# Kernel tuning notes

Hardware: AMD Instinct MI355X
Metric: run time of the kernel (lower is better)

The kernel has to match this reference:

```python
import jax, jax.numpy as jnp
import numpy as np

B, L, D = 16, 512, 512
NPIX, ENC_D = 196, 4096
AL, ATTR_D = 20, 300
H, DK = 8, 64
DFF = 2048
KS = 3


def _lin(x, w, b):
    return x @ w.T + b


def _ln_custom(x, a, b, eps=1e-6):
    # torch .std is unbiased (ddof=1); module divides by (std + eps)
    mean = x.mean(-1, keepdims=True)
    n = x.shape[-1]
    std = jnp.sqrt(((x - mean) ** 2).sum(-1, keepdims=True) / (n - 1))
    return a * (x - mean) / (std + eps) + b


def _ln(x, eps=1e-5):
    # fresh nn.LayerNorm each call -> gamma=1, beta=0
    mean = x.mean(-1, keepdims=True)
    var = ((x - mean) ** 2).mean(-1, keepdims=True)
    return (x - mean) / jnp.sqrt(var + eps)


def _mha(Q, K, V, mask, wq, bq, wk, bk, wv, bv, wo, bo):
    bsz = Q.shape[0]
    q = _lin(Q, wq, bq).reshape(bsz, -1, H, DK)
    k = _lin(K, wk, bk).reshape(bsz, -1, H, DK)
    v = _lin(V, wv, bv).reshape(bsz, -1, H, DK)
    scores = jnp.einsum('bqhd,bkhd->bhqk', q, k) / np.sqrt(DK).astype(np.float32)
    scores = jnp.where(mask[:, None], jnp.float32(-1e9), scores)
    attn = jax.nn.softmax(scores, axis=-1)
    ctx = jnp.einsum('bhqk,bkhd->bqhd', attn, v).reshape(bsz, -1, H * DK)
    out = _lin(ctx, wo, bo)
    return _ln(out + Q), attn


def _lstm_last(xw, w_ih, w_hh, b_ih, b_hh):
    # xw: [N, KS, D]; torch LSTM gate order i,f,g,o; return last hidden
    N = xw.shape[0]
    h = jnp.zeros((N, D), xw.dtype)
    c = jnp.zeros((N, D), xw.dtype)
    for t in range(KS):  # KS=3, unrolled
        g = xw[:, t] @ w_ih.T + b_ih + h @ w_hh.T + b_hh
        i, f, gg, o = jnp.split(g, 4, axis=-1)
        c = jax.nn.sigmoid(f) * c + jax.nn.sigmoid(i) * jnp.tanh(gg)
        h = jax.nn.sigmoid(o) * jnp.tanh(c)
    return h


def _local_rnn(x, conv_w, conv_b, w_ih, w_hh, b_ih, b_hh):
    a, b = jnp.split(x, 2, axis=-1)
    x = a * jax.nn.sigmoid(b)          # GLU: [B,L,512] -> [B,L,256]
    x = x @ conv_w.T + conv_b          # 1x1 conv == linear: -> [B,L,512]
    bsz, l, d = x.shape
    xp = jnp.pad(x, ((0, 0), (KS - 1, 0), (0, 0)))
    win = jnp.stack([xp[:, i:i + l] for i in range(KS)], axis=2)  # [B,L,KS,512]
    h = _lstm_last(win.reshape(-1, KS, d), w_ih, w_hh, b_ih, b_hh)
    return h.reshape(bsz, l, d)


def _forward(dec_inputs, enc_outputs, attr_out,
             dec_self_attn_mask, dec_enc_attn_mask, attr_dec_attn_mask,
             rnn_norm_a, rnn_norm_b, conv_w, conv_b,
             lstm_w_ih, lstm_w_hh, lstm_b_ih, lstm_b_hh,
             sa_wq, sa_bq, sa_wk, sa_bk, sa_wv, sa_bv, sa_wo, sa_bo,
             ea_wq, ea_bq, ea_wk, ea_bk, ea_wv, ea_bv, ea_wo, ea_bo,
             aa_wq, aa_bq, aa_wk, aa_bk, aa_wv, aa_bv, aa_wo, aa_bo,
             fc_w, fc_b, norm_a, norm_b, ffn_w1, ffn_b1, ffn_w2, ffn_b2):
    # LocalRNNLayer: x + local_rnn(custom_LN(x))  (dropout = eval/identity)
    x = dec_inputs + _local_rnn(_ln_custom(dec_inputs, rnn_norm_a, rnn_norm_b),
                                conv_w, conv_b, lstm_w_ih, lstm_w_hh, lstm_b_ih, lstm_b_hh)
    dec_out, self_attn = _mha(x, x, x, dec_self_attn_mask,
                              sa_wq, sa_bq, sa_wk, sa_bk, sa_wv, sa_bv, sa_wo, sa_bo)
    img, enc_attn = _mha(dec_out, enc_outputs, enc_outputs, dec_enc_attn_mask,
                         ea_wq, ea_bq, ea_wk, ea_bk, ea_wv, ea_bv, ea_wo, ea_bo)
    attr, _ = _mha(dec_out, attr_out, attr_out, attr_dec_attn_mask,
                   aa_wq, aa_bq, aa_wk, aa_bk, aa_wv, aa_bv, aa_wo, aa_bo)
    # NOTE: original concatenates img with img (faithful to source bug)
    ct = jax.nn.sigmoid(_lin(jnp.concatenate([img, img], axis=-1), fc_w, fc_b))
    y = _ln_custom(ct * jax.nn.relu(img) + (1.0 - ct) * jax.nn.relu(attr), norm_a, norm_b)
    y = _ln(_lin(jax.nn.relu(_lin(y, ffn_w1, ffn_b1)), ffn_w2, ffn_b2) + y)
    return y, self_attn, enc_attn


def setup_inputs() -> dict:
    key = jax.random.key(0)
    keys = iter(jax.random.split(key, 40))
    w = lambda shape: jax.random.normal(next(keys), shape, jnp.float32) * 0.02
    causal = jnp.broadcast_to(jnp.triu(jnp.ones((L, L), bool), 1), (B, L, L))
    inp = {
        'dec_inputs': jax.random.normal(next(keys), (B, L, D), jnp.float32),
        'enc_outputs': jax.random.normal(next(keys), (B, NPIX, ENC_D), jnp.float32),
        'attr_out': jax.random.normal(next(keys), (B, AL, ATTR_D), jnp.float32),
        'dec_self_attn_mask': causal,
        'dec_enc_attn_mask': jnp.zeros((B, L, NPIX), bool),
        'attr_dec_attn_mask': jnp.zeros((B, L, AL), bool),
        'rnn_norm_a': jnp.ones((D,), jnp.float32),
        'rnn_norm_b': jnp.zeros((D,), jnp.float32),
        'conv_w': w((D, D // 2)), 'conv_b': jnp.zeros((D,), jnp.float32),
        'lstm_w_ih': w((4 * D, D)), 'lstm_w_hh': w((4 * D, D)),
        'lstm_b_ih': jnp.zeros((4 * D,), jnp.float32), 'lstm_b_hh': jnp.zeros((4 * D,), jnp.float32),
        'sa_wq': w((H * DK, D)), 'sa_bq': jnp.zeros((H * DK,), jnp.float32),
        'sa_wk': w((H * DK, D)), 'sa_bk': jnp.zeros((H * DK,), jnp.float32),
        'sa_wv': w((H * DK, D)), 'sa_bv': jnp.zeros((H * DK,), jnp.float32),
        'sa_wo': w((D, H * DK)), 'sa_bo': jnp.zeros((D,), jnp.float32),
        'ea_wq': w((H * DK, D)), 'ea_bq': jnp.zeros((H * DK,), jnp.float32),
        'ea_wk': w((H * DK, ENC_D)), 'ea_bk': jnp.zeros((H * DK,), jnp.float32),
        'ea_wv': w((H * DK, ENC_D)), 'ea_bv': jnp.zeros((H * DK,), jnp.float32),
        'ea_wo': w((D, H * DK)), 'ea_bo': jnp.zeros((D,), jnp.float32),
        'aa_wq': w((H * DK, D)), 'aa_bq': jnp.zeros((H * DK,), jnp.float32),
        'aa_wk': w((H * DK, ATTR_D)), 'aa_bk': jnp.zeros((H * DK,), jnp.float32),
        'aa_wv': w((H * DK, ATTR_D)), 'aa_bv': jnp.zeros((H * DK,), jnp.float32),
        'aa_wo': w((D, H * DK)), 'aa_bo': jnp.zeros((D,), jnp.float32),
        'fc_w': w((D, 2 * D)), 'fc_b': jnp.zeros((D,), jnp.float32),
        'norm_a': jnp.ones((D,), jnp.float32), 'norm_b': jnp.zeros((D,), jnp.float32),
        'ffn_w1': w((DFF, D)), 'ffn_b1': jnp.zeros((DFF,), jnp.float32),
        'ffn_w2': w((D, DFF)), 'ffn_b2': jnp.zeros((D,), jnp.float32),
    }
    return inp


def reference(dec_inputs, enc_outputs, attr_out,
              dec_self_attn_mask, dec_enc_attn_mask, attr_dec_attn_mask,
              rnn_norm_a, rnn_norm_b, conv_w, conv_b,
              lstm_w_ih, lstm_w_hh, lstm_b_ih, lstm_b_hh,
              sa_wq, sa_bq, sa_wk, sa_bk, sa_wv, sa_bv, sa_wo, sa_bo,
              ea_wq, ea_bq, ea_wk, ea_bk, ea_wv, ea_bv, ea_wo, ea_bo,
              aa_wq, aa_bq, aa_wk, aa_bk, aa_wv, aa_bv, aa_wo, aa_bo,
              fc_w, fc_b, norm_a, norm_b, ffn_w1, ffn_b1, ffn_w2, ffn_b2):
    return _forward(dec_inputs, enc_outputs, attr_out,
                    dec_self_attn_mask, dec_enc_attn_mask, attr_dec_attn_mask,
                    rnn_norm_a, rnn_norm_b, conv_w, conv_b,
                    lstm_w_ih, lstm_w_hh, lstm_b_ih, lstm_b_hh,
                    sa_wq, sa_bq, sa_wk, sa_bk, sa_wv, sa_bv, sa_wo, sa_bo,
                    ea_wq, ea_bq, ea_wk, ea_bk, ea_wv, ea_bv, ea_wo, ea_bo,
                    aa_wq, aa_bq, aa_wk, aa_bk, aa_wv, aa_bv, aa_wo, aa_bo,
                    fc_w, fc_b, norm_a, norm_b, ffn_w1, ffn_b1, ffn_w2, ffn_b2)
```

## Files before the change

### kernel.cpp

```cpp
#include <hip/hip_runtime.h>
#include <hip/hip_bf16.h>
#include <math.h>

typedef __hip_bfloat16 bf16;
typedef __attribute__((ext_vector_type(8))) short short8;
typedef __attribute__((ext_vector_type(4))) short short4v;
typedef __attribute__((ext_vector_type(4))) float f32x4;

__device__ __forceinline__ void storef(float* p, float v){ *p = v; }
__device__ __forceinline__ void storef(bf16* p, float v){ *p = __float2bfloat16(v); }
__device__ __forceinline__ float sigm(float x){ return 1.0f/(1.0f+expf(-x)); }
__device__ __forceinline__ float tof(float x){ return x; }
__device__ __forceinline__ float tof(bf16 x){ return __bfloat162float(x); }

__device__ __forceinline__ short f2bs(float f){ bf16 h=__float2bfloat16(f); short s; __builtin_memcpy(&s,&h,2); return s; }
__device__ __forceinline__ void load8(const float* __restrict__ p, short8* dst){
    const f32x4* pp = (const f32x4*)p;
    f32x4 lo = pp[0], hi = pp[1];
    short8 v;
    v[0]=f2bs(lo[0]); v[1]=f2bs(lo[1]); v[2]=f2bs(lo[2]); v[3]=f2bs(lo[3]);
    v[4]=f2bs(hi[0]); v[5]=f2bs(hi[1]); v[6]=f2bs(hi[2]); v[7]=f2bs(hi[3]);
    *dst = v;
}
__device__ __forceinline__ void load8(const bf16* __restrict__ p, short8* dst){
    *dst = *(const short8*)p;
}

__device__ __forceinline__ void gl_lds16(const bf16* g, bf16* l){
    auto gp = (const __attribute__((address_space(1))) unsigned int*)(g);
    auto lp = (__attribute__((address_space(3))) unsigned int*)(l);
    __builtin_amdgcn_global_load_lds(gp, lp, 16, 0, 0);
}

template<int TM, int TN, typename OT, bool RELU, int WSEQ = 0, int WLDT = 0>
__global__ __launch_bounds__(256) void k_gemm_fast(
    const bf16* __restrict__ A, int lda,
    const bf16* __restrict__ B, int ldb,
    OT* __restrict__ C, int ldc,
    const float* __restrict__ bias, int K)
{
    constexpr int FM = TM/32, FN = TN/32;
    __shared__ bf16 As[TM*32];
    __shared__ bf16 Bs[TN*32];
    const int tid = threadIdx.x;
    const int wave = tid >> 6, lane = tid & 63;
    const int m0 = blockIdx.y * TM, n0 = blockIdx.x * TN;
    const int wm = (wave >> 1) * (TM/2), wn = (wave & 1) * (TN/2);
    const int lr = lane & 15, g = lane >> 4;
    const int srow = lane >> 2, sslot = (lane & 3) * 8;
    f32x4 acc[FM][FN] = {};

    for (int k0 = 0; k0 < K; k0 += 32) {
        #pragma unroll
        for (int rd = 0; rd < TM/64; ++rd) {
            int cb = rd*4 + wave;
            gl_lds16(A + (size_t)(m0 + cb*16 + srow)*lda + k0 + sslot, As + cb*512);
        }
        #pragma unroll
        for (int rd = 0; rd < TN/64; ++rd) {
            int cb = rd*4 + wave;
            gl_lds16(B + (size_t)(n0 + cb*16 + srow)*ldb + k0 + sslot, Bs + cb*512);
        }
        __syncthreads();
        short8 af[FM], bf_[FN];
        #pragma unroll
        for (int i = 0; i < FM; ++i) af[i]  = *(const short8*)&As[(wm + i*16 + lr)*32 + g*8];
        #pragma unroll
        for (int j = 0; j < FN; ++j) bf_[j] = *(const short8*)&Bs[(wn + j*16 + lr)*32 + g*8];
        #pragma unroll
        for (int i = 0; i < FM; ++i)
            #pragma unroll
            for (int j = 0; j < FN; ++j)
                acc[i][j] = __builtin_amdgcn_mfma_f32_16x16x32_bf16(af[i], bf_[j], acc[i][j], 0, 0, 0);
        __syncthreads();
    }
    const int cr4 = (lane >> 4) * 4;
    if constexpr (WSEQ > 0) {
        #pragma unroll
        for (int j = 0; j < FN; ++j) {
            int col = n0 + wn + j*16 + lr;
            float bv = bias[col];
            int hh = col >> 6, dd = col & 63;
            #pragma unroll
            for (int i = 0; i < FM; ++i) {
                int r0 = m0 + wm + i*16 + cr4;
                int bb = r0 / WSEQ, ll = r0 % WSEQ;
                short4v pk;
                #pragma unroll
                for (int q = 0; q < 4; ++q) pk[q] = f2bs(acc[i][j][q] + bv);
                *(short4v*)&((bf16*)C)[((size_t)(bb*8 + hh)*64 + dd)*WLDT + ll] = pk;
            }
        }
    } else {
        #pragma unroll
        for (int j = 0; j < FN; ++j) {
            int col = n0 + wn + j*16 + lr;
            float bv = bias[col];
            #pragma unroll
            for (int i = 0; i < FM; ++i) {
                #pragma unroll
                for (int q = 0; q < 4; ++q) {
                    int row = m0 + wm + i*16 + cr4 + q;
                    float v = acc[i][j][q] + bv;
                    if (RELU) v = fmaxf(v, 0.0f);
                    storef(&C[(size_t)row*ldc + col], v);
                }
            }
        }
    }
}

template<int LK, int LKT, bool CAUSAL, bool WPROB, bool VT>
__global__ __launch_bounds__(256) void k_attn(
    const bf16* __restrict__ Q, int ldq, const bf16* __restrict__ K, int ldk,
    const bf16* __restrict__ V, int ldv,
    float* __restrict__ Pout, bf16* __restrict__ ctx)
{
    constexpr int LQ = 512;
    constexpr int NCH = (LK + 63) / 64;
    constexpr int LKP = NCH*64 + 8;
    __shared__ bf16 Qs[32*72];
    __shared__ bf16 Ks[64*72];
    __shared__ bf16 Ps[32*LKP];
    __shared__ float red[4][32];
    const int tid = threadIdx.x, wave = tid >> 6, lane = tid & 63;
    const int lr = lane & 15, g = lane >> 4;
    const int qt = blockIdx.x, bh = blockIdx.y;
    const int b = bh >> 3, h = bh & 7;
    const size_t qbase = (size_t)b*LQ + qt*32;
    const size_t kvbase = (size_t)b*LK;
    {
        int r = tid >> 3, c = (tid & 7) << 3;
        *(short8*)&Qs[r*72 + c] = *(const short8*)&Q[(qbase + r)*ldq + h*64 + c];
    }
    f32x4 acc[2][NCH];
    #pragma unroll
    for (int i = 0; i < 2; ++i)
        #pragma unroll
        for (int j = 0; j < NCH; ++j) acc[i][j] = (f32x4){0,0,0,0};

    for (int ch = 0; ch < NCH; ++ch) {
        __syncthreads();
        #pragma unroll
        for (int i = 0; i < 2; ++i) {
            int idx = tid + i*256;
            int r = idx >> 3, c = (idx & 7) << 3;
            int kr = ch*64 + r;
            short8 v = {};
            if (kr < LK) v = *(const short8*)&K[(kvbase + kr)*ldk + h*64 + c];
            *(short8*)&Ks[r*72 + c] = v;
        }
        __syncthreads();
        #pragma unroll
        for (int kk = 0; kk < 2; ++kk) {
            short8 bf_ = *(const short8*)&Ks[(wave*16 + lr)*72 + kk*32 + g*8];
            #pragma unroll
            for (int mi = 0; mi < 2; ++mi) {
                short8 af = *(const short8*)&Qs[(mi*16 + lr)*72 + kk*32 + g*8];
                acc[mi][ch] = __builtin_amdgcn_mfma_f32_16x16x32_bf16(af, bf_, acc[mi][ch], 0, 0, 0);
            }
        }
    }
    __syncthreads();
    float rmax[2][4];
    #pragma unroll
    for (int mi = 0; mi < 2; ++mi)
        #pragma unroll
        for (int q = 0; q < 4; ++q) {
            int rowg = qt*32 + mi*16 + g*4 + q;
            float m = -INFINITY;
            #pragma unroll
            for (int ch = 0; ch < NCH; ++ch) {
                int col = ch*64 + wave*16 + lr;
                float s = acc[mi][ch][q] * 0.125f;
                if (col >= LK || (CAUSAL && col > rowg)) s = -INFINITY;
                acc[mi][ch][q] = s;
                m = fmaxf(m, s);
            }
            rmax[mi][q] = m;
        }
    #pragma unroll
    for (int off = 1; off < 16; off <<= 1)
        #pragma unroll
        for (int mi = 0; mi < 2; ++mi)
            #pragma unroll
            for (int q = 0; q < 4; ++q)
                rmax[mi][q] = fmaxf(rmax[mi][q], __shfl_xor(rmax[mi][q], off));
    if (lr == 0)
        #pragma unroll
        for (int mi = 0; mi < 2; ++mi)
            #pragma unroll
            for (int q = 0; q < 4; ++q)
                red[wave][mi*16 + g*4 + q] = rmax[mi][q];
    __syncthreads();
    float rsum[2][4];
    #pragma unroll
    for (int mi = 0; mi < 2; ++mi)
        #pragma unroll
        for (int q = 0; q < 4; ++q) {
            int rl = mi*16 + g*4 + q;
            float m = fmaxf(fmaxf(red[0][rl], red[1][rl]), fmaxf(red[2][rl], red[3][rl]));
            float s = 0.0f;
            #pragma unroll
            for (int ch = 0; ch < NCH; ++ch) {
                float e = expf(acc[mi][ch][q] - m);
                acc[mi][ch][q] = e;
                s += e;
            }
            rsum[mi][q] = s;
        }
    #pragma unroll
    for (int off = 1; off < 16; off <<= 1)
        #pragma unroll
        for (int mi = 0; mi < 2; ++mi)
            #pragma unroll
            for (int q = 0; q < 4; ++q)
                rsum[mi][q] += __shfl_xor(rsum[mi][q], off);
    __syncthreads();
    if (lr == 0)
        #pragma unroll
        for (int mi = 0; mi < 2; ++mi)
            #pragma unroll
            for (int q = 0; q < 4; ++q)
                red[wave][mi*16 + g*4 + q] = rsum[mi][q];
    __syncthreads();
    #pragma unroll
    for (int mi = 0; mi < 2; ++mi)
        #pragma unroll
        for (int q = 0; q < 4; ++q) {
            int rl = mi*16 + g*4 + q;
            float inv = 1.0f / (red[0][rl] + red[1][rl] + red[2][rl] + red[3][rl]);
            #pragma unroll
            for (int ch = 0; ch < NCH; ++ch) {
                int col = ch*64 + wave*16 + lr;
                Ps[rl*LKP + col] = __float2bfloat16(acc[mi][ch][q] * inv);
            }
        }
    __syncthreads();
    if (WPROB) {
        const size_t pbase = ((size_t)bh*LQ + qt*32)*LK;
        constexpr int NV = 32*LK/4;
        for (int p = tid; p < NV; p += 256) {
            int e = p*4;
            int row = e / LK, col = e % LK;
            f32x4 v;
            #pragma unroll
            for (int u = 0; u < 4; ++u) v[u] = tof(Ps[row*LKP + col + u]);
            *(f32x4*)&Pout[pbase + (size_t)row*LK + col] = v;
        }
    }
    f32x4 o[2] = {(f32x4){0,0,0,0},(f32x4){0,0,0,0}};
    if constexpr (VT) {
        const bf16* vrow = V + ((size_t)(b*8 + h)*64 + wave*16 + lr)*LKT;
        for (int pc = 0; pc < 2*NCH; ++pc) {
            short8 bf_ = *(const short8*)&vrow[pc*32 + g*8];
            #pragma unroll
            for (int mi = 0; mi < 2; ++mi) {
                short8 af = *(const short8*)&Ps[(mi*16 + lr)*LKP + pc*32 + g*8];
                o[mi] = __builtin_amdgcn_mfma_f32_16x16x32_bf16(af, bf_, o[mi], 0, 0, 0);
            }
        }
    } else {
        short* Vs = (short*)Ks;
        for (int pc = 0; pc < 2*NCH; ++pc) {
            __syncthreads();
            {
                int r = tid >> 3, c = (tid & 7) << 3;
                int kr = pc*32 + r;
                short8 v = {};
                if (kr < LK) v = *(const short8*)&V[(kvbase + kr)*ldv + h*64 + c];
                #pragma unroll
                for (int j = 0; j < 8; ++j) Vs[(c + j)*40 + r] = v[j];
            }
            __syncthreads();
            short8 bf_ = *(const short8*)&Vs[(wave*16 + lr)*40 + g*8];
            #pragma unroll
            for (int mi = 0; mi < 2; ++mi) {
                short8 af = *(const short8*)&Ps[(mi*16 + lr)*LKP + pc*32 + g*8];
                o[mi] = __builtin_amdgcn_mfma_f32_16x16x32_bf16(af, bf_, o[mi], 0, 0, 0);
            }
        }
    }
    const int cr4g = g * 4;
    #pragma unroll
    for (int mi = 0; mi < 2; ++mi)
        #pragma unroll
        for (int q = 0; q < 4; ++q) {
            int rl = mi*16 + cr4g + q;
            storef(&ctx[(qbase + rl)*512 + h*64 + wave*16 + lr], o[mi][q]);
        }
}

struct CvtSeg { const float* src; bf16* dst; };
struct CvtArgs { CvtSeg seg[16]; int cum[17]; int nseg; };
__global__ void k_cvt(CvtArgs a)
{
    int gid = blockIdx.x*256 + threadIdx.x;
    if (gid >= a.cum[a.nseg]) return;
    int s = 0;
    while (s < a.nseg-1 && gid >= a.cum[s+1]) ++s;
    int off = (gid - a.cum[s]) * 8;
    short8 v; load8(a.seg[s].src + off, &v);
    *(short8*)(a.seg[s].dst + off) = v;
}

__global__ void k_cvt_pad(const float* __restrict__ a, const float* __restrict__ wk,
                          const float* __restrict__ wv, bf16* __restrict__ attrp,
                          bf16* __restrict__ kvwp)
{
    int t = blockIdx.x*256 + threadIdx.x;
    if (t >= 1344*320) return;
    int r = t / 320, c = t % 320;
    float v = 0.0f;
    if (c < 300) {
        if (r < 320) v = a[(size_t)r*300 + c];
        else if (r < 832) v = wk[(size_t)(r-320)*300 + c];
        else v = wv[(size_t)(r-832)*300 + c];
    }
    if (r < 320) storef(&attrp[(size_t)r*320 + c], v);
    else storef(&kvwp[(size_t)(r-320)*320 + c], v);
}

__global__ void k_cat2(const float* __restrict__ a, const float* __restrict__ b,
                       float* __restrict__ dst)
{
    int t = blockIdx.x*256 + threadIdx.x;
    if (t < 512) dst[t] = a[t];
    else if (t < 1024) dst[t] = b[t-512];
}

__global__ void k_zero(bf16* __restrict__ p, int n8)
{
    int t = blockIdx.x*256 + threadIdx.x;
    if (t < n8) { short8 z = {}; *(short8*)&p[t*8] = z; }
}

__global__ void k_lnglu(const float* __restrict__ x, const float* __restrict__ a,
                        const float* __restrict__ bpar, bf16* __restrict__ out)
{
    int r = blockIdx.x, tid = threadIdx.x;
    const float* xr = x + (size_t)r*512;
    float v0 = xr[tid], v1 = xr[tid+256];
    __shared__ float red[256];
    red[tid] = v0+v1; __syncthreads();
    for (int s=128;s>0;s>>=1){ if(tid<s) red[tid]+=red[tid+s]; __syncthreads(); }
    float mean = red[0]*(1.0f/512.0f); __syncthreads();
    float d0 = v0-mean, d1 = v1-mean;
    red[tid] = d0*d0+d1*d1; __syncthreads();
    for (int s=128;s>0;s>>=1){ if(tid<s) red[tid]+=red[tid+s]; __syncthreads(); }
    float stdv = sqrtf(red[0]*(1.0f/511.0f));
    float inv = 1.0f/(stdv + 1e-6f);
    float o0 = a[tid]    *d0*inv + bpar[tid];
    float o1 = a[tid+256]*d1*inv + bpar[tid+256];
    storef(&out[(size_t)r*256 + tid], o0 * sigm(o1));
}

__global__ void k_lstm_step(const bf16* __restrict__ XW, const bf16* __restrict__ G,
                            const float* __restrict__ bih, const float* __restrict__ bhh,
                            bf16* __restrict__ h, float* __restrict__ c, int t, int first)
{
    int idx = blockIdx.x*256 + threadIdx.x;
    int n = idx >> 9, j = idx & 511;
    int b = n >> 9, l = n & 511;
    int lp = l - 2 + t;
    float gi, gf, gg, go;
    if (lp >= 0) {
        const bf16* xr = XW + ((size_t)(b*512 + lp))*2048;
        gi = tof(xr[j]); gf = tof(xr[512+j]); gg = tof(xr[1024+j]); go = tof(xr[1536+j]);
    } else {
        gi = bih[j]; gf = bih[512+j]; gg = bih[1024+j]; go = bih[1536+j];
    }
    if (first) {
        gi += bhh[j]; gf += bhh[512+j]; gg += bhh[1024+j]; go += bhh[1536+j];
        float cn = sigm(gi)*tanhf(gg);
        c[idx] = cn;
        storef(&h[idx], sigm(go)*tanhf(cn));
    } else {
        const bf16* gr = G + (size_t)n*2048;
        gi += tof(gr[j]); gf += tof(gr[512+j]); gg += tof(gr[1024+j]); go += tof(gr[1536+j]);
        float cn = sigm(gf)*c[idx] + sigm(gi)*tanhf(gg);
        c[idx] = cn;
        storef(&h[idx], sigm(go)*tanhf(cn));
    }
}

__global__ void k_add(const float* __restrict__ dec, const bf16* __restrict__ h,
                      float* __restrict__ out, bf16* __restrict__ outb)
{
    size_t idx = (size_t)blockIdx.x*256 + threadIdx.x;
    float v = dec[idx] + tof(h[idx]);
    out[idx] = v;
    storef(&outb[idx], v);
}

template<typename RT>
__global__ void k_ln_res(const bf16* __restrict__ x, const RT* __restrict__ res,
                         float* __restrict__ out, bf16* __restrict__ outb, float eps)
{
    int r = blockIdx.x, tid = threadIdx.x;
    const bf16* xr = x + (size_t)r*512;
    const RT* rr = res + (size_t)r*512;
    float v0 = tof(xr[tid]) + tof(rr[tid]), v1 = tof(xr[tid+256]) + tof(rr[tid+256]);
    __shared__ float red[256];
    red[tid] = v0+v1; __syncthreads();
    for (int s=128;s>0;s>>=1){ if(tid<s) red[tid]+=red[tid+s]; __syncthreads(); }
    float mean = red[0]*(1.0f/512.0f); __syncthreads();
    float d0 = v0-mean, d1 = v1-mean;
    red[tid] = d0*d0+d1*d1; __syncthreads();
    for (int s=128;s>0;s>>=1){ if(tid<s) red[tid]+=red[tid+s]; __syncthreads(); }
    float inv = rsqrtf(red[0]*(1.0f/512.0f) + eps);
    float o0 = d0*inv, o1 = d1*inv;
    out[(size_t)r*512 + tid]     = o0;
    out[(size_t)r*512 + tid+256] = o1;
    if (outb) {
        storef(&outb[(size_t)r*512 + tid],     o0);
        storef(&outb[(size_t)r*512 + tid+256], o1);
    }
}

__global__ void k_gate_ln(const bf16* __restrict__ ctpre, const float* __restrict__ img,
                          const float* __restrict__ attr, const float* __restrict__ na,
                          const float* __restrict__ nb, bf16* __restrict__ out)
{
    int r = blockIdx.x, tid = threadIdx.x;
    size_t base = (size_t)r*512;
    float ct0 = sigm(tof(ctpre[base+tid]));
    float v0 = ct0*fmaxf(img[base+tid],0.f) + (1.f-ct0)*fmaxf(attr[base+tid],0.f);
    float ct1 = sigm(tof(ctpre[base+tid+256]));
    float v1 = ct1*fmaxf(img[base+tid+256],0.f) + (1.f-ct1)*fmaxf(attr[base+tid+256],0.f);
    __shared__ float red[256];
    red[tid] = v0+v1; __syncthreads();
    for (int s=128;s>0;s>>=1){ if(tid<s) red[tid]+=red[tid+s]; __syncthreads(); }
    float mean = red[0]*(1.0f/512.0f); __syncthreads();
    float d0 = v0-mean, d1 = v1-mean;
    red[tid] = d0*d0+d1*d1; __syncthreads();
    for (int s=128;s>0;s>>=1){ if(tid<s) red[tid]+=red[tid+s]; __syncthreads(); }
    float stdv = sqrtf(red[0]*(1.0f/511.0f));
    float inv = 1.0f/(stdv + 1e-6f);
    storef(&out[base+tid],     na[tid]    *d0*inv + nb[tid]);
    storef(&out[base+tid+256], na[tid+256]*d1*inv + nb[tid+256]);
}

__global__ void k_fold(const float* __restrict__ fcw, bf16* __restrict__ fold)
{
    int idx = blockIdx.x*256 + threadIdx.x;
    int d = idx >> 9, j = idx & 511;
    storef(&fold[idx], fcw[(size_t)d*1024 + j] + fcw[(size_t)d*1024 + 512 + j]);
}

extern "C" void kernel_launch(void* const* d_in, const int* in_sizes, int n_in,
                              void* d_out, int out_size, void* d_ws, size_t ws_size,
                              hipStream_t stream)
{
    const float* dec_inputs  = (const float*)d_in[0];
    const float* enc_outputs = (const float*)d_in[1];
    const float* attr_out    = (const float*)d_in[2];
    const float* rnn_a  = (const float*)d_in[6];
    const float* rnn_b  = (const float*)d_in[7];
    const float* conv_w = (const float*)d_in[8];
    const float* conv_b = (const float*)d_in[9];
    const float* w_ih   = (const float*)d_in[10];
    const float* w_hh   = (const float*)d_in[11];
    const float* b_ih   = (const float*)d_in[12];
    const float* b_hh   = (const float*)d_in[13];
    const float* sa_wq  = (const float*)d_in[14]; const float* sa_bq = (const float*)d_in[15];
    const float* sa_wk  = (const float*)d_in[16]; const float* sa_bk = (const float*)d_in[17];
    const float* sa_wv  = (const float*)d_in[18]; const float* sa_bv = (const float*)d_in[19];
    const float* sa_wo  = (const float*)d_in[20]; const float* sa_bo = (const float*)d_in[21];
    const float* ea_wq  = (const float*)d_in[22]; const float* ea_bq = (const float*)d_in[23];
    const float* ea_wk  = (const float*)d_in[24]; const float* ea_bk = (const float*)d_in[25];
    const float* ea_wv  = (const float*)d_in[26]; const float* ea_bv = (const float*)d_in[27];
    const float* ea_wo  = (const float*)d_in[28]; const float* ea_bo = (const float*)d_in[29];
    const float* aa_wq  = (const float*)d_in[30]; const float* aa_bq = (const float*)d_in[31];
    const float* aa_wk  = (const float*)d_in[32]; const float* aa_bk = (const float*)d_in[33];
    const float* aa_wv  = (const float*)d_in[34]; const float* aa_bv = (const float*)d_in[35];
    const float* aa_wo  = (const float*)d_in[36]; const float* aa_bo = (const float*)d_in[37];
    const float* fc_w   = (const float*)d_in[38]; const float* fc_b  = (const float*)d_in[39];
    const float* norm_a = (const float*)d_in[40]; const float* norm_b= (const float*)d_in[41];
    const float* ffn_w1 = (const float*)d_in[42]; const float* ffn_b1= (const float*)d_in[43];
    const float* ffn_w2 = (const float*)d_in[44]; const float* ffn_b2= (const float*)d_in[45];

    float* out_y  = (float*)d_out;
    float* out_sa = out_y + 4194304ull;
    float* out_ea = out_sa + 33554432ull;

    bf16* xwb = (bf16*)out_sa;
    bf16* gb  = xwb + 16777216ull;
    bf16* wA  = (bf16*)(out_sa + 16777216ull);
    bf16* conv_wb = wA;
    bf16* w_ihb   = conv_wb + 131072;
    bf16* w_hhb   = w_ihb + 1048576;
    bf16* sa_wqb  = w_hhb + 1048576;
    bf16* sa_wkb  = sa_wqb + 262144;
    bf16* sa_wvb  = sa_wkb + 262144;
    bf16* enc_b   = (bf16*)out_ea;
    bf16* ea_wkb  = (bf16*)(out_ea + 6422528ull);
    bf16* ea_wvb  = ea_wkb + 2097152;

    char* W = (char*)d_ws;
    float* S0 = (float*)(W);
    float* S1 = (float*)(W + (16ull<<20));
    float* S2 = (float*)(W + (32ull<<20));
    bf16*  T0 = (bf16*) (W + (48ull<<20));
    bf16*  T1 = (bf16*) (W + (56ull<<20));
    bf16*  T2 = (bf16*) (W + (64ull<<20));
    bf16*  T3 = (bf16*) (W + (72ull<<20));
    bf16*  glufb = (bf16*)(W + (80ull<<20));
    bf16*  hb    = (bf16*)(W + (80ull<<20));
    bf16*  dec_out_b = (bf16*)(W + (88ull<<20));
    bf16*  img_b     = (bf16*)(W + (96ull<<20));
    bf16*  wsW   = (bf16*)(W + (104ull<<20));
    bf16* ea_wqb = wsW;
    bf16* aa_wqb = ea_wqb + 262144;
    bf16* ea_wob = aa_wqb + 262144;
    bf16* aa_wob = ea_wob + 262144;
    bf16* sa_wob = aa_wob + 262144;
    bf16* foldb  = sa_wob + 262144;
    bf16* ffn_w1b = foldb + 262144;
    bf16* ffn_w2b = ffn_w1b + 1048576;
    float* bqk_self = (float*)(W + (112ull<<20));
    float* bq_eaaa  = bqk_self + 1024;
    float* b_attrkv = bq_eaaa + 1024;
    bf16* midb = (bf16*)S1;
    bf16* kenc   = (bf16*)S0;
    bf16* vt_enc = (bf16*)(W + (4ull<<20));
    bf16* kvattr = (bf16*)(W + (8ull<<20));
    bf16* attrp  = (bf16*)(W + (10ull<<20));
    bf16* kvwp   = (bf16*)(W + (11ull<<20));

    {
        CvtArgs ca;
        const float* srcs[16] = {conv_w, w_ih, w_hh, sa_wq, sa_wk, sa_wv, sa_wo, ea_wq,
                                 aa_wq, ea_wo, aa_wo, ffn_w1, ffn_w2, ea_wk, ea_wv, enc_outputs};
        bf16* dsts[16] = {conv_wb, w_ihb, w_hhb, sa_wqb, sa_wkb, sa_wvb, sa_wob, ea_wqb,
                          aa_wqb, ea_wob, aa_wob, ffn_w1b, ffn_w2b, ea_wkb, ea_wvb, enc_b};
        int ns[16] = {131072, 1048576, 1048576, 262144, 262144, 262144, 262144, 262144,
                      262144, 262144, 262144, 1048576, 1048576, 2097152, 2097152, 12845056};
        int cum = 0;
        for (int i = 0; i < 16; ++i) { ca.seg[i] = {srcs[i], dsts[i]}; ca.cum[i] = cum; cum += ns[i]/8; }
        ca.cum[16] = cum; ca.nseg = 16;
        k_cvt<<<(cum + 255)/256, 256, 0, stream>>>(ca);
    }
    k_fold<<<1024,256,0,stream>>>(fc_w, foldb);
    k_cat2<<<4,256,0,stream>>>(sa_bq, sa_bk, bqk_self);
    k_cat2<<<4,256,0,stream>>>(ea_bq, aa_bq, bq_eaaa);
    k_cat2<<<4,256,0,stream>>>(aa_bk, aa_bv, b_attrkv);

    dim3 gP(4,128), gPQ(8,128), gX(16,64), gE(4,49), gA(16,128);

    k_lnglu<<<8192,256,0,stream>>>(dec_inputs, rnn_a, rnn_b, glufb);
    k_gemm_fast<64,128,bf16,false><<<gP,256,0,stream>>>(glufb,256, conv_wb,256, T0,512, conv_b, 256);
    k_gemm_fast<128,128,bf16,false><<<gX,256,0,stream>>>(T0,512, w_ihb,512, xwb,2048, b_ih, 512);
    k_lstm_step<<<16384,256,0,stream>>>(xwb, nullptr, b_ih, b_hh, hb, S2, 0, 1);
    k_gemm_fast<128,128,bf16,false><<<gX,256,0,stream>>>(hb,512, w_hhb,512, gb,2048, b_hh, 512);
    k_lstm_step<<<16384,256,0,stream>>>(xwb, gb, b_ih, b_hh, hb, S2, 1, 0);
    k_gemm_fast<128,128,bf16,false><<<gX,256,0,stream>>>(hb,512, w_hhb,512, gb,2048, b_hh, 512);
    k_lstm_step<<<16384,256,0,stream>>>(xwb, gb, b_ih, b_hh, hb, S2, 2, 0);
    k_add<<<16384,256,0,stream>>>(dec_inputs, hb, S0, hb);

    k_gemm_fast<64,128,bf16,false><<<gPQ,256,0,stream>>>(hb,512, sa_wqb,512, T0,1024, bqk_self, 512);
    k_gemm_fast<64,128,bf16,false,512,512><<<gP,256,0,stream>>>(hb,512, sa_wvb,512, T2,0, sa_bv, 512);
    k_attn<512,512,true,true,true><<<gA,256,0,stream>>>(T0,1024, T0+512,1024, T2,0, out_sa, T3);
    k_gemm_fast<64,128,bf16,false><<<gP,256,0,stream>>>(T3,512, sa_wob,512, T1,512, sa_bo, 512);
    k_ln_res<float><<<8192,256,0,stream>>>(T1, S0, S1, dec_out_b, 1e-5f);

    k_zero<<<1024,256,0,stream>>>(vt_enc, 262144);
    k_gemm_fast<64,128,bf16,false><<<gPQ,256,0,stream>>>(dec_out_b,512, ea_wqb,512, T0,1024, bq_eaaa, 512);
    k_gemm_fast<64,128,bf16,false><<<gE,256,0,stream>>>(enc_b,4096, ea_wkb,4096, kenc,512, ea_bk, 4096);
    k_gemm_fast<64,128,bf16,false,196,256><<<gE,256,0,stream>>>(enc_b,4096, ea_wvb,4096, vt_enc,0, ea_bv, 4096);
    k_attn<196,256,false,true,true><<<gA,256,0,stream>>>(T0,1024, kenc,512, vt_enc,0, out_ea, T3);
    k_gemm_fast<64,128,bf16,false><<<gP,256,0,stream>>>(T3,512, ea_wob,512, T2,512, ea_bo, 512);
    k_ln_res<float><<<8192,256,0,stream>>>(T2, S1, S2, img_b, 1e-5f);

    k_cvt_pad<<<1680,256,0,stream>>>(attr_out, aa_wk, aa_wv, attrp, kvwp);
    { dim3 ga(8,5,1);
      k_gemm_fast<64,128,bf16,false><<<ga,256,0,stream>>>(attrp,320, kvwp,320, kvattr,1024, b_attrkv, 320); }
    k_attn<20,20,false,false,false><<<gA,256,0,stream>>>(T0+512,1024, kvattr,1024, kvattr+512,1024, nullptr, T3);
    k_gemm_fast<64,128,bf16,false><<<gP,256,0,stream>>>(T3,512, aa_wob,512, T2,512, aa_bo, 512);
    k_ln_res<float><<<8192,256,0,stream>>>(T2, S1, S0, nullptr, 1e-5f);

    k_gemm_fast<64,128,bf16,false><<<gP,256,0,stream>>>(img_b,512, foldb,512, T0,512, fc_b, 512);
    k_gate_ln<<<8192,256,0,stream>>>(T0, S2, S0, norm_a, norm_b, T2);
    k_gemm_fast<128,128,bf16,true><<<gX,256,0,stream>>>(T2,512, ffn_w1b,512, midb,2048, ffn_b1, 512);
    k_gemm_fast<64,128,bf16,false><<<gP,256,0,stream>>>(midb,2048, ffn_w2b,2048, T1,512, ffn_b2, 2048);
    k_ln_res<bf16><<<8192,256,0,stream>>>(T1, T2, out_y, nullptr, 1e-5f);
}
```

Before: 786.4 us.

## Fuse QKV and encoder K/V projections into single GEMMs; fuse last LSTM step with residual

```diff
diff --git a/kernel.cpp b/kernel.cpp
--- a/kernel.cpp
+++ b/kernel.cpp
@@ -32,11 +32,11 @@
     __builtin_amdgcn_global_load_lds(gp, lp, 16, 0, 0);
 }
 
-template<int TM, int TN, typename OT, bool RELU, int WSEQ = 0, int WLDT = 0>
+template<int TM, int TN, typename OT, bool RELU, int WSEQ = 0, int WLDT = 0, int WCUT = 0>
 __global__ __launch_bounds__(256) void k_gemm_fast(
     const bf16* __restrict__ A, int lda,
     const bf16* __restrict__ B, int ldb,
-    OT* __restrict__ C, int ldc,
+    OT* __restrict__ C, int ldc, bf16* __restrict__ C2,
     const float* __restrict__ bias, int K)
 {
     constexpr int FM = TM/32, FN = TN/32;
@@ -75,12 +75,13 @@
         __syncthreads();
     }
     const int cr4 = (lane >> 4) * 4;
-    if constexpr (WSEQ > 0) {
-        #pragma unroll
-        for (int j = 0; j < FN; ++j) {
-            int col = n0 + wn + j*16 + lr;
-            float bv = bias[col];
-            int hh = col >> 6, dd = col & 63;
+    #pragma unroll
+    for (int j = 0; j < FN; ++j) {
+        int col = n0 + wn + j*16 + lr;
+        float bv = bias[col];
+        if (WSEQ > 0 && col >= WCUT) {
+            int colv = col - WCUT;
+            int hh = colv >> 6, dd = colv & 63;
             #pragma unroll
             for (int i = 0; i < FM; ++i) {
                 int r0 = m0 + wm + i*16 + cr4;
@@ -88,14 +89,9 @@
                 short4v pk;
                 #pragma unroll
                 for (int q = 0; q < 4; ++q) pk[q] = f2bs(acc[i][j][q] + bv);
-                *(short4v*)&((bf16*)C)[((size_t)(bb*8 + hh)*64 + dd)*WLDT + ll] = pk;
-            }
-        }
-    } else {
-        #pragma unroll
-        for (int j = 0; j < FN; ++j) {
-            int col = n0 + wn + j*16 + lr;
-            float bv = bias[col];
+                *(short4v*)&C2[((size_t)(bb*8 + hh)*64 + dd)*WLDT + ll] = pk;
+            }
+        } else {
             #pragma unroll
             for (int i = 0; i < FM; ++i) {
                 #pragma unroll
@@ -329,6 +325,15 @@
     else if (t < 1024) dst[t] = b[t-512];
 }
 
+__global__ void k_cat3(const float* __restrict__ a, const float* __restrict__ b,
+                       const float* __restrict__ c, float* __restrict__ dst)
+{
+    int t = blockIdx.x*256 + threadIdx.x;
+    if (t < 512) dst[t] = a[t];
+    else if (t < 1024) dst[t] = b[t-512];
+    else if (t < 1536) dst[t] = c[t-1024];
+}
+
 __global__ void k_zero(bf16* __restrict__ p, int n8)
 {
     int t = blockIdx.x*256 + threadIdx.x;
@@ -384,13 +389,22 @@
     }
 }
 
-__global__ void k_add(const float* __restrict__ dec, const bf16* __restrict__ h,
-                      float* __restrict__ out, bf16* __restrict__ outb)
-{
-    size_t idx = (size_t)blockIdx.x*256 + threadIdx.x;
-    float v = dec[idx] + tof(h[idx]);
-    out[idx] = v;
-    storef(&outb[idx], v);
+__global__ void k_lstm_last(const bf16* __restrict__ XW, const bf16* __restrict__ G,
+                            const float* __restrict__ dec, const float* __restrict__ c,
+                            float* __restrict__ x1f, bf16* __restrict__ x1b)
+{
+    int idx = blockIdx.x*256 + threadIdx.x;
+    int n = idx >> 9, j = idx & 511;
+    int b = n >> 9, l = n & 511;
+    const bf16* xr = XW + ((size_t)(b*512 + l))*2048;
+    float gi = tof(xr[j]), gf = tof(xr[512+j]), gg = tof(xr[1024+j]), go = tof(xr[1536+j]);
+    const bf16* gr = G + (size_t)n*2048;
+    gi += tof(gr[j]); gf += tof(gr[512+j]); gg += tof(gr[1024+j]); go += tof(gr[1536+j]);
+    float cn = sigm(gf)*c[idx] + sigm(gi)*tanhf(gg);
+    float h = sigm(go)*tanhf(cn);
+    float v = dec[idx] + h;
+    x1f[idx] = v;
+    storef(&x1b[idx], v);
 }
 
 template<typename RT>
@@ -518,9 +532,10 @@
     bf16* foldb  = sa_wob + 262144;
     bf16* ffn_w1b = foldb + 262144;
     bf16* ffn_w2b = ffn_w1b + 1048576;
-    float* bqk_self = (float*)(W + (112ull<<20));
-    float* bq_eaaa  = bqk_self + 1024;
+    float* b_qkv    = (float*)(W + (112ull<<20));
+    float* bq_eaaa  = b_qkv + 1536;
     float* b_attrkv = bq_eaaa + 1024;
+    float* b_enckv  = b_attrkv + 1024;
     bf16* midb = (bf16*)S1;
     bf16* kenc   = (bf16*)S0;
     bf16* vt_enc = (bf16*)(W + (4ull<<20));
@@ -542,46 +557,46 @@
         k_cvt<<<(cum + 255)/256, 256, 0, stream>>>(ca);
     }
     k_fold<<<1024,256,0,stream>>>(fc_w, foldb);
-    k_cat2<<<4,256,0,stream>>>(sa_bq, sa_bk, bqk_self);
+    k_cat3<<<6,256,0,stream>>>(sa_bq, sa_bk, sa_bv, b_qkv);
     k_cat2<<<4,256,0,stream>>>(ea_bq, aa_bq, bq_eaaa);
     k_cat2<<<4,256,0,stream>>>(aa_bk, aa_bv, b_attrkv);
-
-    dim3 gP(4,128), gPQ(8,128), gX(16,64), gE(4,49), gA(16,128);
+    k_cat2<<<4,256,0,stream>>>(ea_bk, ea_bv, b_enckv);
+
+    dim3 gP(4,128), gPQ(8,128), gQKV(12,128), gX(16,64), gEKV(8,49), gA(16,128);
 
     k_lnglu<<<8192,256,0,stream>>>(dec_inputs, rnn_a, rnn_b, glufb);
-    k_gemm_fast<64,128,bf16,false><<<gP,256,0,stream>>>(glufb,256, conv_wb,256, T0,512, conv_b, 256);
-    k_gemm_fast<128,128,bf16,false><<<gX,256,0,stream>>>(T0,512, w_ihb,512, xwb,2048, b_ih, 512);
+    k_gemm_fast<64,128,bf16,false><<<gP,256,0,stream>>>(glufb,256, conv_wb,256, T0,512, nullptr, conv_b, 256);
+    k_gemm_fast<128,128,bf16,false><<<gX,256,0,stream>>>(T0,512, w_ihb,512, xwb,2048, nullptr, b_ih, 512);
     k_lstm_step<<<16384,256,0,stream>>>(xwb, nullptr, b_ih, b_hh, hb, S2, 0, 1);
-    k_gemm_fast<128,128,bf16,false><<<gX,256,0,stream>>>(hb,512, w_hhb,512, gb,2048, b_hh, 512);
+    k_gemm_fast<128,128,bf16,false><<<gX,256,0,stream>>>(hb,512, w_hhb,512, gb,2048, nullptr, b_hh, 512);
     k_lstm_step<<<16384,256,0,stream>>>(xwb, gb, b_ih, b_hh, hb, S2, 1, 0);
-    k_gemm_fast<128,128,bf16,false><<<gX,256,0,stream>>>(hb,512, w_hhb,512, gb,2048, b_hh, 512);
-    k_lstm_step<<<16384,256,0,stream>>>(xwb, gb, b_ih, b_hh, hb, S2, 2, 0);
-    k_add<<<16384,256,0,stream>>>(dec_inputs, hb, S0, hb);
-
-    k_gemm_fast<64,128,bf16,false><<<gPQ,256,0,stream>>>(hb,512, sa_wqb,512, T0,1024, bqk_self, 512);
-    k_gemm_fast<64,128,bf16,false,512,512><<<gP,256,0,stream>>>(hb,512, sa_wvb,512, T2,0, sa_bv, 512);
+    k_gemm_fast<128,128,bf16,false><<<gX,256,0,stream>>>(hb,512, w_hhb,512, gb,2048, nullptr, b_hh, 512);
+    k_lstm_last<<<16384,256,0,stream>>>(xwb, gb, dec_inputs, S2, S0, hb);
+
+    k_gemm_fast<64,128,bf16,false,512,512,1024><<<gQKV,256,0,stream>>>(
+        hb,512, sa_wqb,512, T0,1024, T2, b_qkv, 512);
     k_attn<512,512,true,true,true><<<gA,256,0,stream>>>(T0,1024, T0+512,1024, T2,0, out_sa, T3);
-    k_gemm_fast<64,128,bf16,false><<<gP,256,0,stream>>>(T3,512, sa_wob,512, T1,512, sa_bo, 512);
+    k_gemm_fast<64,128,bf16,false><<<gP,256,0,stream>>>(T3,512, sa_wob,512, T1,512, nullptr, sa_bo, 512);
     k_ln_res<float><<<8192,256,0,stream>>>(T1, S0, S1, dec_out_b, 1e-5f);
 
     k_zero<<<1024,256,0,stream>>>(vt_enc, 262144);
-    k_gemm_fast<64,128,bf16,false><<<gPQ,256,0,stream>>>(dec_out_b,512, ea_wqb,512, T0,1024, bq_eaaa, 512);
-    k_gemm_fast<64,128,bf16,false><<<gE,256,0,stream>>>(enc_b,4096, ea_wkb,4096, kenc,512, ea_bk, 4096);
-    k_gemm_fast<64,128,bf16,false,196,256><<<gE,256,0,stream>>>(enc_b,4096, ea_wvb,4096, vt_enc,0, ea_bv, 4096);
+    k_gemm_fast<64,128,bf16,false><<<gPQ,256,0,stream>>>(dec_out_b,512, ea_wqb,512, T0,1024, nullptr, bq_eaaa, 512);
+    k_gemm_fast<64,128,bf16,false,196,256,512><<<gEKV,256,0,stream>>>(
+        enc_b,4096, ea_wkb,4096, kenc,512, vt_enc, b_enckv, 4096);
     k_attn<196,256,false,true,true><<<gA,256,0,stream>>>(T0,1024, kenc,512, vt_enc,0, out_ea, T3);
-    k_gemm_fast<64,128,bf16,false><<<gP,256,0,stream>>>(T3,512, ea_wob,512, T2,512, ea_bo, 512);
+    k_gemm_fast<64,128,bf16,false><<<gP,256,0,stream>>>(T3,512, ea_wob,512, T2,512, nullptr, ea_bo, 512);
     k_ln_res<float><<<8192,256,0,stream>>>(T2, S1, S2, img_b, 1e-5f);
 
     k_cvt_pad<<<1680,256,0,stream>>>(attr_out, aa_wk, aa_wv, attrp, kvwp);
     { dim3 ga(8,5,1);
-      k_gemm_fast<64,128,bf16,false><<<ga,256,0,stream>>>(attrp,320, kvwp,320, kvattr,1024, b_attrkv, 320); }
+      k_gemm_fast<64,128,bf16,false><<<ga,256,0,stream>>>(attrp,320, kvwp,320, kvattr,1024, nullptr, b_attrkv, 320); }
     k_attn<20,20,false,false,false><<<gA,256,0,stream>>>(T0+512,1024, kvattr,1024, kvattr+512,1024, nullptr, T3);
-    k_gemm_fast<64,128,bf16,false><<<gP,256,0,stream>>>(T3,512, aa_wob,512, T2,512, aa_bo, 512);
+    k_gemm_fast<64,128,bf16,false><<<gP,256,0,stream>>>(T3,512, aa_wob,512, T2,512, nullptr, aa_bo, 512);
     k_ln_res<float><<<8192,256,0,stream>>>(T2, S1, S0, nullptr, 1e-5f);
 
-    k_gemm_fast<64,128,bf16,false><<<gP,256,0,stream>>>(img_b,512, foldb,512, T0,512, fc_b, 512);
+    k_gemm_fast<64,128,bf16,false><<<gP,256,0,stream>>>(img_b,512, foldb,512, T0,512, nullptr, fc_b, 512);
     k_gate_ln<<<8192,256,0,stream>>>(T0, S2, S0, norm_a, norm_b, T2);
-    k_gemm_fast<128,128,bf16,true><<<gX,256,0,stream>>>(T2,512, ffn_w1b,512, midb,2048, ffn_b1, 512);
-    k_gemm_fast<64,128,bf16,false><<<gP,256,0,stream>>>(midb,2048, ffn_w2b,2048, T1,512, ffn_b2, 2048);
+    k_gemm_fast<128,128,bf16,true><<<gX,256,0,stream>>>(T2,512, ffn_w1b,512, midb,2048, nullptr, ffn_b1, 512);
+    k_gemm_fast<64,128,bf16,false><<<gP,256,0,stream>>>(midb,2048, ffn_w2b,2048, T1,512, nullptr, ffn_b2, 2048);
     k_ln_res<bf16><<<8192,256,0,stream>>>(T1, T2, out_y, nullptr, 1e-5f);
 }
```

New measurement: 700.8 us. -10.9%, faster.
